# Performance work log

Measured on AMD Instinct MI355X. Metric: run time of the kernel, lower is better.

Reference implementation:

```python
import jax, jax.numpy as jnp
import numpy as np
from jax import lax

KERNEL = 3      # patch size
STRIDE = 1      # matching stride at low res
RATE = 2        # downsample rate
SOFTMAX_SCALE = 10.0


def _extract_patches(img, k, stride):
    """tf.image.extract_patches with SAME padding. img: [B,H,W,C] -> [B, oh*ow, k, k, C]."""
    B, H, W, C = img.shape
    oh = -(-H // stride)
    ow = -(-W // stride)
    ph = max((oh - 1) * stride + k - H, 0)
    pw = max((ow - 1) * stride + k - W, 0)
    img = jnp.pad(img, ((0, 0), (ph // 2, ph - ph // 2), (pw // 2, pw - pw // 2), (0, 0)))
    # stack the k*k shifted strided views; channel-last order matches TF's (kh, kw, C) flattening
    cols = [img[:, dh:dh + (oh - 1) * stride + 1:stride, dw:dw + (ow - 1) * stride + 1:stride, :]
            for dh in range(k) for dw in range(k)]
    p = jnp.stack(cols, axis=3)  # [B, oh, ow, k*k, C]
    return p.reshape(B, oh * ow, k, k, C)


def _avgpool2(x):
    """Exact equivalent of TF bilinear (antialias=False) downsample by factor 2."""
    B, H, W, C = x.shape
    return x.reshape(B, H // 2, 2, W // 2, 2, C).mean(axis=(2, 4))


def _conv_same(x4, w):
    return lax.conv_general_dilated(x4, w, (1, 1), 'SAME',
                                    dimension_numbers=('NHWC', 'HWIO', 'NHWC'))


def _forward(x, mask):
    B, H, W, C = x.shape
    k, stride, rate = KERNEL, STRIDE, RATE
    h, w = H // rate, W // rate
    L = h * w

    # raw (full-res) patches used for reconstruction: [B,k,k,C,L]
    raw_w = jnp.transpose(_extract_patches(x, k, rate * stride), (0, 2, 3, 4, 1))
    # low-res foreground / background (identical here, as in the source)
    f = _avgpool2(x)              # [B,h,w,C]
    m = _avgpool2(mask)           # [B,h,w,1]
    # low-res matching patches: [B,k,k,C,L]
    wp = jnp.transpose(_extract_patches(f, k, stride), (0, 2, 3, 4, 1))
    # mask patches -> gate: mm = 1 where the 3x3 mask patch mean is exactly 1.0
    mp = _extract_patches(m, k, stride)                       # [B,L,k,k,1]
    mm = (jnp.mean(mp, axis=(2, 3, 4)) == 1.0).astype(jnp.float32)  # [B,L]

    fuse_w = jnp.eye(KERNEL, dtype=jnp.float32).reshape(KERNEL, KERNEL, 1, 1)

    def per_item(xi, wi, rwi, mmi):
        # xi:[h,w,C]  wi,rwi:[k,k,C,L]  mmi:[L]
        wn = wi / jnp.maximum(jnp.sqrt(jnp.sum(wi * wi, axis=(0, 1, 2))), 1e-4)
        yi = _conv_same(xi[None], wn)          # [1,h,w,L] cosine-similarity logits
        att = yi[0]
        # fuse: diagonal conv over the [L,L] score matrix in both patch orderings
        z = yi.reshape(1, L, L, 1)
        z = _conv_same(z, fuse_w)
        z = z.reshape(1, h, w, h, w).transpose(0, 2, 1, 4, 3).reshape(1, L, L, 1)
        z = _conv_same(z, fuse_w)
        z = z.reshape(1, w, h, w, h).transpose(0, 2, 1, 4, 3)
        yi = z.reshape(1, h, w, L)
        mm4 = mmi.reshape(1, 1, 1, L)
        yi = jax.nn.softmax(yi * mm4 * SOFTMAX_SCALE, axis=3) * mm4
        # reconstruction: transposed conv with raw full-res patches as filters
        out = lax.conv_transpose(yi, rwi, (rate, rate), 'SAME',
                                 dimension_numbers=('NHWC', 'HWIO', 'NHWC'),
                                 transpose_kernel=True) / float(rate * rate)
        return out[0], att

    y, att = jax.vmap(per_item)(f, wp, raw_w, mm)
    return y, att


def setup_inputs() -> dict:
    key = jax.random.key(0)
    x = jax.random.normal(key, (2, 128, 128, 64), dtype=jnp.float32)
    # binary hole mask: ones inside a centered 64x64 square
    mask = jnp.zeros((2, 128, 128, 1), jnp.float32).at[:, 32:96, 32:96, :].set(1.0)
    return {"x": x, "mask": mask}


def reference(x, mask):
    return _forward(x, mask)
```

## Files before the change

kernel.cpp:

```cpp
#include <hip/hip_runtime.h>
#include <hip/hip_bf16.h>

typedef _Float16 f16x8 __attribute__((ext_vector_type(8)));
typedef float f32x4 __attribute__((ext_vector_type(4)));

__device__ __forceinline__ void gload_lds16(const void* gptr, void* lptr) {
  __builtin_amdgcn_global_load_lds(
      (const __attribute__((address_space(1))) void*)gptr,
      (__attribute__((address_space(3))) void*)lptr, 16, 0, 0);
}

__global__ __launch_bounds__(256) void k_prt(const float* __restrict__ x,
                                             const float* __restrict__ mask,
                                             _Float16* __restrict__ f_h,
                                             float* __restrict__ sumsq,
                                             float* __restrict__ mlow,
                                             _Float16* __restrict__ Rt) {
  if (blockIdx.x < 2048) {
    int wave = threadIdx.x >> 6, c = threadIdx.x & 63;
    int blk = blockIdx.x * 4 + wave;
    int b = blk >> 12, ij = blk & 4095;
    int i = ij >> 6, j = ij & 63;
    size_t base = ((size_t)(b * 128 + 2 * i) * 128 + 2 * j) * 64 + c;
    float f = 0.25f * (x[base] + x[base + 64] + x[base + 128 * 64] + x[base + 128 * 64 + 64]);
    f_h[(size_t)blk * 64 + c] = (_Float16)f;
    float fsq = f * f;
    for (int off = 32; off; off >>= 1) fsq += __shfl_down(fsq, off);
    if (c == 0) {
      sumsq[blk] = fsq;
      size_t mb = (size_t)(b * 128 + 2 * i) * 128 + 2 * j;
      mlow[blk] = 0.25f * (mask[mb] + mask[mb + 1] + mask[mb + 128] + mask[mb + 129]);
    }
    return;
  }
  int idx = blockIdx.x - 2048;
  int kh = idx % 3;
  int rest = idx / 3;
  int li = rest & 63, b = rest >> 6;
  int r = 2 * li + kh;
  __shared__ float xrow[128 * 65];
  if (r < 128) {
    for (int t = threadIdx.x; t < 8192; t += 256) {
      int v = t >> 6, c = t & 63;
      xrow[v * 65 + c] = x[((size_t)(b * 128 + r) * 128 + v) * 64 + c];
    }
  }
  __syncthreads();
  for (int id2 = threadIdx.x; id2 < 12288; id2 += 256) {
    int lj = id2 & 63, rest2 = id2 >> 6;
    int c = rest2 & 63, kw = rest2 >> 6;
    int v = 2 * lj + kw;
    float val = (r < 128 && v < 128) ? xrow[v * 65 + c] : 0.f;
    int n = (kh * 3 + kw) * 64 + c;
    Rt[((size_t)b * 640 + n) * 4096 + li * 64 + lj] = (_Float16)val;
  }
}

__global__ __launch_bounds__(1024) void k_norm_compact(const float* __restrict__ sumsq,
                                                       const float* __restrict__ mlow,
                                                       float* __restrict__ invn,
                                                       int* __restrict__ actIdx,
                                                       int* __restrict__ nAct) {
  int b = blockIdx.x;
  int t = threadIdx.x;
  __shared__ unsigned char mmf[4096];
  for (int l = t; l < 4096; l += 1024) {
    int li = l >> 6, lj = l & 63;
    float s = 0.f;
    bool ok = true;
    for (int dh = -1; dh <= 1; ++dh)
      for (int dw = -1; dw <= 1; ++dw) {
        int ii = li + dh, jj = lj + dw;
        float mv = 0.f;
        if ((unsigned)ii < 64u && (unsigned)jj < 64u) {
          int idx = (b << 12) + ii * 64 + jj;
          s += sumsq[idx];
          mv = mlow[idx];
        }
        ok = ok && (mv == 1.0f);
      }
    invn[(b << 12) + l] = 1.0f / fmaxf(sqrtf(s), 1e-4f);
    mmf[l] = ok ? 1 : 0;
  }
  __syncthreads();
  int lane = t & 63, wv = t >> 6;
  __shared__ int wsum[16];
  __shared__ int sbase;
  if (t == 0) sbase = 0;
  __syncthreads();
  for (int chunk = 0; chunk < 4; ++chunk) {
    int l = chunk * 1024 + t;
    int flag = mmf[l] ? 1 : 0;
    unsigned long long m = __ballot(flag);
    int wpre = __popcll(m & ((1ull << lane) - 1ull));
    if (lane == 0) wsum[wv] = __popcll(m);
    __syncthreads();
    int off = sbase;
    for (int w2 = 0; w2 < wv; ++w2) off += wsum[w2];
    if (flag) {
      int pos = off + wpre;
      if (pos < 1024) actIdx[(b << 10) + pos] = l;
    }
    __syncthreads();
    if (t == 0) {
      int s2 = 0;
      for (int w2 = 0; w2 < 16; ++w2) s2 += wsum[w2];
      sbase += s2;
    }
    __syncthreads();
  }
  int total = sbase;
  if (t >= total) actIdx[(b << 10) + t] = 0;
  if (t == 0) nAct[b] = (total > 1024) ? 1024 : total;
}

__global__ __launch_bounds__(256) void k_psub(const _Float16* __restrict__ f_h,
                                              _Float16* __restrict__ P,
                                              const _Float16* __restrict__ Rt,
                                              const int* __restrict__ actIdx,
                                              _Float16* __restrict__ Rts) {
  if (blockIdx.x < 2048) {
    int wave = threadIdx.x >> 6, c = threadIdx.x & 63;
    int blk = blockIdx.x * 4 + wave;
    int b = blk >> 12, l = blk & 4095;
    int li = l >> 6, lj = l & 63;
    _Float16* dst = P + (size_t)blk * 576 + c;
#pragma unroll
    for (int kk = 0; kk < 9; ++kk) {
      int kh = kk / 3, kw = kk % 3;
      int ii = li + kh - 1, jj = lj + kw - 1;
      _Float16 v = (_Float16)0.f;
      if ((unsigned)ii < 64u && (unsigned)jj < 64u)
        v = f_h[((size_t)(b << 12) + ii * 64 + jj) * 64 + c];
      dst[kk * 64] = v;
    }
    return;
  }
  int idx = blockIdx.x - 2048;
  int n = idx % 640, b = idx / 640;
  const _Float16* src = Rt + ((size_t)b * 640 + n) * 4096;
  _Float16* dst = Rts + ((size_t)b * 640 + n) * 1024;
  const int* aIdx = actIdx + (b << 10);
  for (int s = threadIdx.x; s < 1024; s += 256) dst[s] = src[aIdx[s]];
}

__global__ __launch_bounds__(256) void k_gemm_sim(const _Float16* __restrict__ P,
                                                  const float* __restrict__ invn,
                                                  float* __restrict__ att) {
  int b = blockIdx.z;
  const _Float16* Ab = P + (size_t)b * 4096 * 576;
  int idx = blockIdx.x;
  int bj = (int)((sqrtf(8.f * (float)idx + 1.f) - 1.f) * 0.5f);
  while ((bj + 1) * (bj + 2) / 2 <= idx) ++bj;
  while (bj * (bj + 1) / 2 > idx) --bj;
  int bi = idx - bj * (bj + 1) / 2;
  int rowBase = bi * 128, colBase = bj * 128;
  bool diag = (bi == bj);

  __shared__ alignas(16) _Float16 As[128 * 64];
  __shared__ alignas(16) _Float16 Bs[128 * 64];
  __shared__ alignas(16) float tbuf[32][132];
  int tid = threadIdx.x, wave = tid >> 6, lane = tid & 63;
  int q = lane >> 4, rr = lane & 15;
  int wr = (wave >> 1) * 64, wc = (wave & 1) * 64;
  f32x4 acc[4][4] = {};
  for (int kt = 0; kt < 576; kt += 64) {
    __syncthreads();
#pragma unroll
    for (int t = 0; t < 4; ++t) {
      int chunk = t * 256 + wave * 64 + lane;
      int row = chunk >> 3;
      int kc = ((chunk & 7) ^ (row & 7)) * 8;
      gload_lds16(Ab + (size_t)(rowBase + row) * 576 + kt + kc,
                  As + (size_t)(t * 256 + wave * 64) * 8);
      if (!diag)
        gload_lds16(Ab + (size_t)(colBase + row) * 576 + kt + kc,
                    Bs + (size_t)(t * 256 + wave * 64) * 8);
    }
    __syncthreads();
    const _Float16* Bsrc = diag ? As : Bs;
#pragma unroll
    for (int ks = 0; ks < 2; ++ks) {
      f16x8 af[4], bf[4];
#pragma unroll
      for (int mi = 0; mi < 4; ++mi) {
        int r = wr + mi * 16 + rr;
        int ps = (ks * 4 + q) ^ (r & 7);
        af[mi] = *(const f16x8*)(As + r * 64 + ps * 8);
      }
#pragma unroll
      for (int ni = 0; ni < 4; ++ni) {
        int r = wc + ni * 16 + rr;
        int ps = (ks * 4 + q) ^ (r & 7);
        bf[ni] = *(const f16x8*)(Bsrc + r * 64 + ps * 8);
      }
#pragma unroll
      for (int mi = 0; mi < 4; ++mi)
#pragma unroll
        for (int ni = 0; ni < 4; ++ni)
          acc[mi][ni] = __builtin_amdgcn_mfma_f32_16x16x32_f16(af[mi], bf[ni], acc[mi][ni], 0, 0, 0);
    }
  }
  float* attb = att + ((size_t)b << 24);
#pragma unroll
  for (int ni = 0; ni < 4; ++ni) {
    int gc = colBase + wc + ni * 16 + rr;
    float sc = invn[(b << 12) + gc];
#pragma unroll
    for (int mi = 0; mi < 4; ++mi)
#pragma unroll
      for (int reg = 0; reg < 4; ++reg) {
        int gr = rowBase + wr + mi * 16 + q * 4 + reg;
        attb[((size_t)gr << 12) + gc] = acc[mi][ni][reg] * sc;
      }
  }
  if (diag) return;
  const float* ivrow = invn + (b << 12) + rowBase;
#pragma unroll
  for (int ph = 0; ph < 4; ++ph) {
    __syncthreads();
    if ((ph >> 1) == (wc >> 6)) {
      int nlo = (ph & 1) * 2;
#pragma unroll
      for (int nn = 0; nn < 2; ++nn) {
        int ni = nlo + nn;
        int rloc = nn * 16 + rr;
#pragma unroll
        for (int mi = 0; mi < 4; ++mi)
          *(f32x4*)&tbuf[rloc][wr + mi * 16 + q * 4] = acc[mi][ni];
      }
    }
    __syncthreads();
    int r = tid >> 3;
    int cbase = (tid & 7) * 16;
    int grow = colBase + ph * 32 + r;
    float* dst = attb + ((size_t)grow << 12) + rowBase + cbase;
#pragma unroll
    for (int cc = 0; cc < 16; cc += 4) {
      f32x4 v = *(f32x4*)&tbuf[r][cbase + cc];
      f32x4 s = *(const f32x4*)(ivrow + cbase + cc);
      *(f32x4*)(dst + cc) = v * s;
    }
  }
}

__global__ __launch_bounds__(256) void k_fuse_softmax3(const float* __restrict__ att,
                                                       const int* __restrict__ actIdx,
                                                       const int* __restrict__ nAct,
                                                       _Float16* __restrict__ Asub) {
  int blk0 = blockIdx.x;
  int blk = (blk0 & 7) * 1024 + (blk0 >> 3);
  int b = blk >> 12, p = blk & 4095;
  const float* Y = att + ((size_t)b << 24);
  const int* aIdx = actIdx + (b << 10);
  int na = nAct[b];
  int tid = threadIdx.x;
  int pi = p >> 6, pj = p & 63;
  int acol = pj * 64 + pi;

  int ls[4];
  bool act[4];
  float F[4] = {0.f, 0.f, 0.f, 0.f};
#pragma unroll
  for (int s4 = 0; s4 < 4; ++s4) {
    int slot = s4 * 256 + tid;
    ls[s4] = aIdx[slot];
    act[s4] = (slot < na);
  }

#pragma unroll
  for (int d2 = -1; d2 <= 1; ++d2) {
    int a2 = acol + d2;
    if ((unsigned)a2 >= 4096u) continue;
    int p2 = ((a2 & 63) << 6) | (a2 >> 6);
    int l2[4];
    bool lok[4];
#pragma unroll
    for (int s4 = 0; s4 < 4; ++s4) {
      int l = ls[s4];
      int bcol = ((l & 63) << 6) | (l >> 6);
      int b2 = bcol + d2;
      lok[s4] = act[s4] && ((unsigned)b2 < 4096u);
      int b2c = lok[s4] ? b2 : 0;
      l2[s4] = ((b2c & 63) << 6) | (b2c >> 6);
    }
#pragma unroll
    for (int d1 = -1; d1 <= 1; ++d1) {
      int qq = p2 + d1;
      if ((unsigned)qq >= 4096u) continue;
      const float* row = Y + ((size_t)qq << 12);
#pragma unroll
      for (int s4 = 0; s4 < 4; ++s4) {
        int rr2 = l2[s4] + d1;
        if (lok[s4] && (unsigned)rr2 < 4096u) F[s4] += row[rr2];
      }
    }
  }

  float z[4];
  float mx = (na < 4096) ? 0.f : -1e30f;
#pragma unroll
  for (int s4 = 0; s4 < 4; ++s4) {
    z[s4] = act[s4] ? F[s4] * 10.f : -1e30f;
    mx = fmaxf(mx, z[s4]);
  }
  __shared__ float red[4];
  for (int off = 32; off; off >>= 1) mx = fmaxf(mx, __shfl_down(mx, off));
  if ((tid & 63) == 0) red[tid >> 6] = mx;
  __syncthreads();
  mx = fmaxf(fmaxf(red[0], red[1]), fmaxf(red[2], red[3]));
  float e[4];
  float esum = 0.f;
#pragma unroll
  for (int s4 = 0; s4 < 4; ++s4) {
    e[s4] = act[s4] ? __expf(z[s4] - mx) : 0.f;
    esum += e[s4];
  }
  for (int off = 32; off; off >>= 1) esum += __shfl_down(esum, off);
  __syncthreads();
  if ((tid & 63) == 0) red[tid >> 6] = esum;
  __syncthreads();
  float total = red[0] + red[1] + red[2] + red[3] + (float)(4096 - na) * __expf(0.f - mx);
  float inv = 1.f / total;
  _Float16* Ap = Asub + ((size_t)blk << 10);
#pragma unroll
  for (int s4 = 0; s4 < 4; ++s4) Ap[s4 * 256 + tid] = (_Float16)(e[s4] * inv);
}

__global__ __launch_bounds__(256) void k_gemm_recon(const _Float16* __restrict__ Asub,
                                                    const _Float16* __restrict__ Rts,
                                                    float* __restrict__ y) {
  int b = blockIdx.z;
  const _Float16* Ab = Asub + ((size_t)b << 22);
  const _Float16* Bb = Rts + (size_t)b * 640 * 1024;
  int rowBase = blockIdx.y * 128, colBase = blockIdx.x * 128;
  __shared__ alignas(16) _Float16 As[128 * 64];
  __shared__ alignas(16) _Float16 Bs[128 * 64];
  int tid = threadIdx.x, wave = tid >> 6, lane = tid & 63;
  int q = lane >> 4, rr = lane & 15;
  int wr = (wave >> 1) * 64, wc = (wave & 1) * 64;
  f32x4 acc[4][4] = {};
  for (int kt = 0; kt < 1024; kt += 64) {
    __syncthreads();
#pragma unroll
    for (int t = 0; t < 4; ++t) {
      int chunk = t * 256 + wave * 64 + lane;
      int row = chunk >> 3;
      int kc = ((chunk & 7) ^ (row & 7)) * 8;
      gload_lds16(Ab + ((size_t)(rowBase + row) << 10) + kt + kc,
                  As + (size_t)(t * 256 + wave * 64) * 8);
      gload_lds16(Bb + ((size_t)(colBase + row) << 10) + kt + kc,
                  Bs + (size_t)(t * 256 + wave * 64) * 8);
    }
    __syncthreads();
#pragma unroll
    for (int ks = 0; ks < 2; ++ks) {
      f16x8 af[4], bf[4];
#pragma unroll
      for (int mi = 0; mi < 4; ++mi) {
        int r = wr + mi * 16 + rr;
        int ps = (ks * 4 + q) ^ (r & 7);
        af[mi] = *(const f16x8*)(As + r * 64 + ps * 8);
      }
#pragma unroll
      for (int ni = 0; ni < 4; ++ni) {
        int r = wc + ni * 16 + rr;
        int ps = (ks * 4 + q) ^ (r & 7);
        bf[ni] = *(const f16x8*)(Bs + r * 64 + ps * 8);
      }
#pragma unroll
      for (int mi = 0; mi < 4; ++mi)
#pragma unroll
        for (int ni = 0; ni < 4; ++ni)
          acc[mi][ni] = __builtin_amdgcn_mfma_f32_16x16x32_f16(af[mi], bf[ni], acc[mi][ni], 0, 0, 0);
    }
  }
#pragma unroll
  for (int ni = 0; ni < 4; ++ni) {
    int gc = colBase + wc + ni * 16 + rr;
    if (gc < 576) {
      int kk = gc >> 6, c = gc & 63;
      int kh = kk / 3, kw = kk - kh * 3;
#pragma unroll
      for (int mi = 0; mi < 4; ++mi)
#pragma unroll
        for (int reg = 0; reg < 4; ++reg) {
          int gp = rowBase + wr + mi * 16 + q * 4 + reg;
          int i = gp >> 6, j = gp & 63;
          int u = 2 * i + kh, v = 2 * j + kw;
          if (u < 128 && v < 128)
            atomicAdd(y + (((size_t)((b * 128 + u) * 128 + v)) << 6) + c,
                      0.25f * acc[mi][ni][reg]);
        }
    }
  }
}

extern "C" void kernel_launch(void* const* d_in, const int* in_sizes, int n_in,
                              void* d_out, int out_size, void* d_ws, size_t ws_size,
                              hipStream_t stream) {
  const float* x = (const float*)d_in[0];
  const float* mask = (const float*)d_in[1];
  float* out = (float*)d_out;
  float* y = out;
  float* att = out + 2097152;

  char* ws = (char*)d_ws;
  _Float16* f_h = (_Float16*)(ws + 0);
  float* sumsq = (float*)(ws + 0x100000);
  float* mlow = (float*)(ws + 0x108000);
  float* invn = (float*)(ws + 0x110000);
  _Float16* P = (_Float16*)(ws + 0x120000);
  _Float16* Rt = (_Float16*)(ws + 0xA20000);
  int* actIdx = (int*)(ws + 0x1420000);
  int* nAct = (int*)(ws + 0x1422000);
  _Float16* Rts = (_Float16*)(ws + 0x1430000);
  _Float16* Asub = (_Float16*)(ws + 0x16B0000);
  (void)in_sizes; (void)n_in; (void)out_size; (void)ws_size;

  hipMemsetAsync(y, 0, (size_t)2097152 * 4, stream);

  k_prt<<<2432, 256, 0, stream>>>(x, mask, f_h, sumsq, mlow, Rt);
  k_norm_compact<<<2, 1024, 0, stream>>>(sumsq, mlow, invn, actIdx, nAct);
  k_psub<<<3328, 256, 0, stream>>>(f_h, P, Rt, actIdx, Rts);
  k_gemm_sim<<<dim3(528, 1, 2), 256, 0, stream>>>(P, invn, att);
  k_fuse_softmax3<<<8192, 256, 0, stream>>>(att, actIdx, nAct, Asub);
  k_gemm_recon<<<dim3(5, 32, 2), 256, 0, stream>>>(Asub, Rts, y);
}
```

Before: 295.4 us.

## Fuse y zeroing into prep kernel, vectorize gather, swizzle sim blocks, trim recon K

Replaces the separate memset of y with extra blocks in the first prep kernel that write zeros as vector stores. The Rts gather now packs four f16 values into one 64-bit store per thread. The similarity GEMM remaps block indices for better cache locality and writes att with nontemporal stores. The reconstruction GEMM limits its K loop to the active count rounded up to 64. Together these target launch overhead, store efficiency, cache pollution and wasted MFMA work on zero-padded columns. The K trim assumes Asub and Rts entries past nAct are zero or irrelevant.

Measured after the change: 394.1 us. 1.33x slower.

```diff
diff --git a/kernel.cpp b/kernel.cpp
--- a/kernel.cpp
+++ b/kernel.cpp
@@ -15,7 +15,8 @@
                                              _Float16* __restrict__ f_h,
                                              float* __restrict__ sumsq,
                                              float* __restrict__ mlow,
-                                             _Float16* __restrict__ Rt) {
+                                             _Float16* __restrict__ Rt,
+                                             float* __restrict__ y) {
   if (blockIdx.x < 2048) {
     int wave = threadIdx.x >> 6, c = threadIdx.x & 63;
     int blk = blockIdx.x * 4 + wave;
@@ -31,6 +32,14 @@
       size_t mb = (size_t)(b * 128 + 2 * i) * 128 + 2 * j;
       mlow[blk] = 0.25f * (mask[mb] + mask[mb + 1] + mask[mb + 128] + mask[mb + 129]);
     }
+    return;
+  }
+  if (blockIdx.x >= 2432) {
+    int idx = blockIdx.x - 2432;
+    f32x4* Y4 = (f32x4*)y;
+    f32x4 z = {0.f, 0.f, 0.f, 0.f};
+#pragma unroll
+    for (int k = 0; k < 4; ++k) Y4[idx * 1024 + k * 256 + threadIdx.x] = z;
     return;
   }
   int idx = blockIdx.x - 2048;
@@ -138,10 +147,15 @@
   }
   int idx = blockIdx.x - 2048;
   int n = idx % 640, b = idx / 640;
-  const _Float16* src = Rt + ((size_t)b * 640 + n) * 4096;
+  const unsigned short* src = (const unsigned short*)(Rt + ((size_t)b * 640 + n) * 4096);
   _Float16* dst = Rts + ((size_t)b * 640 + n) * 1024;
   const int* aIdx = actIdx + (b << 10);
-  for (int s = threadIdx.x; s < 1024; s += 256) dst[s] = src[aIdx[s]];
+  int s0 = threadIdx.x * 4;
+  unsigned long long v = (unsigned long long)src[aIdx[s0]] |
+                         ((unsigned long long)src[aIdx[s0 + 1]] << 16) |
+                         ((unsigned long long)src[aIdx[s0 + 2]] << 32) |
+                         ((unsigned long long)src[aIdx[s0 + 3]] << 48);
+  *(unsigned long long*)(dst + s0) = v;
 }
 
 __global__ __launch_bounds__(256) void k_gemm_sim(const _Float16* __restrict__ P,
@@ -149,7 +163,8 @@
                                                   float* __restrict__ att) {
   int b = blockIdx.z;
   const _Float16* Ab = P + (size_t)b * 4096 * 576;
-  int idx = blockIdx.x;
+  int idx0 = blockIdx.x;
+  int idx = (idx0 & 7) * 66 + (idx0 >> 3);
   int bj = (int)((sqrtf(8.f * (float)idx + 1.f) - 1.f) * 0.5f);
   while ((bj + 1) * (bj + 2) / 2 <= idx) ++bj;
   while (bj * (bj + 1) / 2 > idx) --bj;
@@ -211,7 +226,8 @@
 #pragma unroll
       for (int reg = 0; reg < 4; ++reg) {
         int gr = rowBase + wr + mi * 16 + q * 4 + reg;
-        attb[((size_t)gr << 12) + gc] = acc[mi][ni][reg] * sc;
+        __builtin_nontemporal_store(acc[mi][ni][reg] * sc,
+                                    attb + ((size_t)gr << 12) + gc);
       }
   }
   if (diag) return;
@@ -239,7 +255,7 @@
     for (int cc = 0; cc < 16; cc += 4) {
       f32x4 v = *(f32x4*)&tbuf[r][cbase + cc];
       f32x4 s = *(const f32x4*)(ivrow + cbase + cc);
-      *(f32x4*)(dst + cc) = v * s;
+      __builtin_nontemporal_store(v * s, (f32x4*)(dst + cc));
     }
   }
 }
@@ -329,10 +345,12 @@
 
 __global__ __launch_bounds__(256) void k_gemm_recon(const _Float16* __restrict__ Asub,
                                                     const _Float16* __restrict__ Rts,
+                                                    const int* __restrict__ nAct,
                                                     float* __restrict__ y) {
   int b = blockIdx.z;
   const _Float16* Ab = Asub + ((size_t)b << 22);
   const _Float16* Bb = Rts + (size_t)b * 640 * 1024;
+  int kMax = ((nAct[b] + 63) >> 6) << 6;
   int rowBase = blockIdx.y * 128, colBase = blockIdx.x * 128;
   __shared__ alignas(16) _Float16 As[128 * 64];
   __shared__ alignas(16) _Float16 Bs[128 * 64];
@@ -340,7 +358,7 @@
   int q = lane >> 4, rr = lane & 15;
   int wr = (wave >> 1) * 64, wc = (wave & 1) * 64;
   f32x4 acc[4][4] = {};
-  for (int kt = 0; kt < 1024; kt += 64) {
+  for (int kt = 0; kt < kMax; kt += 64) {
     __syncthreads();
 #pragma unroll
     for (int t = 0; t < 4; ++t) {
@@ -418,12 +436,10 @@
   _Float16* Asub = (_Float16*)(ws + 0x16B0000);
   (void)in_sizes; (void)n_in; (void)out_size; (void)ws_size;
 
-  hipMemsetAsync(y, 0, (size_t)2097152 * 4, stream);
-
-  k_prt<<<2432, 256, 0, stream>>>(x, mask, f_h, sumsq, mlow, Rt);
+  k_prt<<<2944, 256, 0, stream>>>(x, mask, f_h, sumsq, mlow, Rt, y);
   k_norm_compact<<<2, 1024, 0, stream>>>(sumsq, mlow, invn, actIdx, nAct);
   k_psub<<<3328, 256, 0, stream>>>(f_h, P, Rt, actIdx, Rts);
   k_gemm_sim<<<dim3(528, 1, 2), 256, 0, stream>>>(P, invn, att);
   k_fuse_softmax3<<<8192, 256, 0, stream>>>(att, actIdx, nAct, Asub);
-  k_gemm_recon<<<dim3(5, 32, 2), 256, 0, stream>>>(Asub, Rts, y);
-}
+  k_gemm_recon<<<dim3(5, 32, 2), 256, 0, stream>>>(Asub, Rts, nAct, y);
+}
```
